# Kernel tuning notes

Hardware: AMD Instinct MI355X
Metric: run time of the kernel (lower is better)

## Reference

```python
import jax, jax.numpy as jnp
import numpy as np
from jax import lax

DN = ('NCHW', 'OIHW', 'NCHW')

def _winit(key, fan_in, shape):
    return (jax.random.uniform(key, shape) - 0.5) * 2 * 2.4 / fan_in ** 0.5

def setup_inputs() -> dict:
    key = jax.random.key(0)
    ks = jax.random.split(key, 6)
    B = 131072
    x = jax.random.normal(ks[0], (B, 1, 16, 16), dtype=jnp.float32)
    H1w = _winit(ks[1], 5 * 5 * 1, (12, 1, 5, 5))
    H1b = jnp.zeros((12, 8, 8), jnp.float32)
    H2w = _winit(ks[2], 5 * 5 * 8, (12, 8, 5, 5))
    H2b = jnp.zeros((12, 4, 4), jnp.float32)
    H3w = _winit(ks[3], 4 * 4 * 12, (4 * 4 * 12, 30))
    H3b = jnp.zeros((30,), jnp.float32)
    outw = _winit(ks[4], 30, (30, 10))
    outb = jnp.zeros((10,), jnp.float32)
    return {"x": x, "H1w": H1w, "H1b": H1b, "H2w": H2w, "H2b": H2b,
            "H3w": H3w, "H3b": H3b, "outw": outw, "outb": outb}

def _pad_m1(x):
    # constant pad of 2 on H and W with value -1.0
    return jnp.pad(x, ((0, 0), (0, 0), (2, 2), (2, 2)), constant_values=-1.0)

def _conv_s2(x, w):
    return lax.conv_general_dilated(x, w, window_strides=(2, 2),
                                    padding='VALID', dimension_numbers=DN)

def reference(x, H1w, H1b, H2w, H2b, H3w, H3b, outw, outb):
    # eval mode: no roll augmentation, dropout is identity
    x = _pad_m1(x)                                   # [B,1,20,20]
    x = _conv_s2(x, H1w) + H1b                       # [B,12,8,8]
    x = jax.nn.relu(x)
    x = _pad_m1(x)                                   # [B,12,12,12]
    s1 = _conv_s2(x[:, 0:8], H2w[0:4])               # [B,4,4,4]
    s2 = _conv_s2(x[:, 4:12], H2w[4:8])              # [B,4,4,4]
    s3 = _conv_s2(jnp.concatenate((x[:, 0:4], x[:, 8:12]), axis=1), H2w[8:12])
    x = jnp.concatenate((s1, s2, s3), axis=1) + H2b  # [B,12,4,4]
    x = jax.nn.relu(x)
    x = x.reshape(x.shape[0], -1)                    # [B,192]
    x = jax.nn.relu(x @ H3w + H3b)                   # [B,30]
    return x @ outw + outb                           # [B,10]
```

## Files before the change

### kernel.cpp

```cpp
#include <hip/hip_runtime.h>
#include <hip/hip_fp16.h>

typedef _Float16 f16x8 __attribute__((ext_vector_type(8)));
typedef float f32x4 __attribute__((ext_vector_type(4)));

union U4H8 { uint4 u; f16x8 h; };
__device__ inline f16x8 asH(uint4 u){ U4H8 x; x.u = u; return x.h; }
__device__ inline unsigned int pk(float a, float b){
    __half2 h = __floats2half2_rn(a, b);
    union { __half2 h; unsigned int u; } c; c.h = h; return c.u;
}
__device__ inline unsigned int pkr(float a, float b){
    return pk(fmaxf(a, 0.f), fmaxf(b, 0.f));
}
__device__ inline unsigned short h16(float a){
    union { __half h; unsigned short s; } c; c.h = __float2half(a); return c.s;
}

#define NFRAG 28
#define WS_B1 7168
#define WS_B2 8192
#define WS_B3 8448
#define WS_B4 8960

__global__ __launch_bounds__(256) void build_tables(
    const float* __restrict__ H1w, const float* __restrict__ H1b,
    const float* __restrict__ H2w, const float* __restrict__ H2b,
    const float* __restrict__ H3w, const float* __restrict__ H3b,
    const float* __restrict__ outw, const float* __restrict__ outb,
    unsigned int* __restrict__ ws)
{
    const int t = threadIdx.x, b = blockIdx.x;
    float* wsf = (float*)ws;

    if (b < NFRAG) {
        if (t < 64) {
            const int lane = t, ch = lane >> 4, oc = lane & 15;
            const int fi = b;
            unsigned short us[8];
            for (int j = 0; j < 8; ++j) {
                float w = 0.f;
                if (fi < 2) {
                    int kh = fi * 4 + ch;
                    if (kh < 5 && j < 5 && oc < 12) w = H1w[oc * 25 + kh * 5 + j];
                } else if (fi < 15) {
                    int kk = fi - 2;
                    int tap = kk * 2 + (ch >> 1);
                    int ic = (ch & 1) * 8 + j;
                    if (tap < 25 && oc < 12) {
                        int kh = tap / 5, kw = tap % 5;
                        int q = oc >> 2, icl = -1;
                        if (q == 0)      { if (ic < 8) icl = ic; }
                        else if (q == 1) { if (ic >= 4 && ic < 12) icl = ic - 4; }
                        else             { if (ic < 4) icl = ic;
                                           else if (ic >= 8 && ic < 12) icl = ic - 4; }
                        if (icl >= 0) w = H2w[((oc * 8 + icl) * 5 + kh) * 5 + kw];
                    }
                } else if (fi < 27) {
                    int idx = fi - 15, nt = idx / 6, kk = idx % 6;
                    int k = kk * 32 + ch * 8 + j;
                    int pos = k / 12, oc2 = k % 12;
                    int col = nt * 16 + oc;
                    if (col < 30) w = H3w[(oc2 * 16 + pos) * 30 + col];
                } else {
                    int k = ch * 8 + j;
                    if (k < 30 && oc < 10) w = outw[k * 10 + oc];
                }
                us[j] = h16(w);
            }
            uint4 u;
            u.x = us[0] | ((unsigned int)us[1] << 16);
            u.y = us[2] | ((unsigned int)us[3] << 16);
            u.z = us[4] | ((unsigned int)us[5] << 16);
            u.w = us[6] | ((unsigned int)us[7] << 16);
            ((uint4*)ws)[fi * 64 + lane] = u;
        }
    } else if (b == NFRAG) {
        for (int idx = t; idx < 1024; idx += 256) {
            int e = idx >> 6, l2 = idx & 63;
            int tt = e >> 2, r = e & 3;
            int oc = 4 * (l2 >> 4) + r, m2 = l2 & 15;
            int oh = 2 * tt + (m2 >> 3), ow = m2 & 7;
            float v = 0.f;
            if (oc < 12) {
                v = H1b[oc * 64 + oh * 8 + ow];
                for (int kh = 0; kh < 5; ++kh)
                    for (int kw = 0; kw < 5; ++kw) {
                        int rr = 2 * oh + kh, cc = 2 * ow + kw;
                        if (rr < 2 || rr >= 18 || cc < 2 || cc >= 18)
                            v -= H1w[oc * 25 + kh * 5 + kw];
                    }
            }
            wsf[WS_B1 + e * 64 + l2] = v;
        }
    } else {
        {
            int e = t >> 6, l2 = t & 63;
            int oc = 4 * (l2 >> 4) + e, m2 = l2 & 15;
            int oh = m2 >> 2, ow = m2 & 3;
            float v = 0.f;
            if (oc < 12) {
                v = H2b[oc * 16 + oh * 4 + ow];
                for (int icl = 0; icl < 8; ++icl)
                    for (int kh = 0; kh < 5; ++kh)
                        for (int kw = 0; kw < 5; ++kw) {
                            int rr = 2 * oh + kh - 2, cc = 2 * ow + kw - 2;
                            if (rr < 0 || rr >= 8 || cc < 0 || cc >= 8)
                                v -= H2w[((oc * 8 + icl) * 5 + kh) * 5 + kw];
                        }
            }
            wsf[WS_B2 + e * 64 + l2] = v;
        }
        for (int i = t; i < 512; i += 256) {
            int e = i >> 6, l2 = i & 63;
            int nt = e >> 2, r = e & 3, ch = l2 >> 4;
            int j = nt * 16 + 4 * ch + r;
            wsf[WS_B3 + e * 64 + l2] = (j < 30) ? H3b[j] : 0.f;
        }
        {
            int e = t >> 6, l2 = t & 63, ch = l2 >> 4;
            int j = 4 * ch + e;
            wsf[WS_B4 + e * 64 + l2] = (j < 10) ? outb[j] : 0.f;
        }
    }
}

#define H2B 18432
#define H3B 21504
__global__ __launch_bounds__(256, 4) void modernnet_mfma(
    const float* __restrict__ x, const unsigned int* __restrict__ ws,
    float* __restrict__ out)
{
    __shared__ uint4 lds4[1376];
    char* L = (char*)lds4;
    const int t = threadIdx.x, wave = t >> 6, l = t & 63;
    const int ch = l >> 4, m = l & 15;
    char* base = L + wave * 4608;
    const int sblk = blockIdx.x * 8;
    const int s0 = sblk + wave * 2;

    const uint4* fr = (const uint4*)ws;
    const float* wsf = (const float*)ws;

    float4 xv0 = *(const float4*)(x + (size_t)(s0 + 0) * 256 + l * 4);
    float4 xv1 = *(const float4*)(x + (size_t)(s0 + 1) * 256 + l * 4);

    uint4 c1b0 = fr[0 * 64 + l], c1b1 = fr[1 * 64 + l];
    f32x4 b1f[4];
    #pragma unroll
    for (int tt = 0; tt < 4; ++tt)
        #pragma unroll
        for (int r = 0; r < 4; ++r) b1f[tt][r] = wsf[WS_B1 + (tt * 4 + r) * 64 + l];

    int c2off[13];
    {
        const int mb = 24 * (m >> 2) + 2 * (m & 3);
        const int hb = (ch & 1) << 4;
        const int sel = (ch >> 1) & 1;
        #pragma unroll
        for (int kk = 0; kk < 13; ++kk) {
            const int t0 = 2 * kk;
            const int t1 = (2 * kk + 1 <= 24) ? 2 * kk + 1 : 24;
            const int p0 = (t0 / 5) * 12 + (t0 % 5);
            const int p1 = (t1 / 5) * 12 + (t1 % 5);
            int pos = mb + (sel ? p1 : p0);
            c2off[kk] = ((pos << 5) + hb) ^ ((pos & 12) << 2);
        }
    }

    uint4 c2b[13];
    #pragma unroll
    for (int kk = 0; kk < 13; ++kk) c2b[kk] = fr[(2 + kk) * 64 + l];
    f32x4 b2f;
    #pragma unroll
    for (int r = 0; r < 4; ++r) b2f[r] = wsf[WS_B2 + r * 64 + l];

    #pragma unroll
    for (int s = 0; s < 2; ++s) {
        {
            uint4 z; z.x = z.y = z.z = z.w = 0u;
            if (l < 60) ((uint4*)base)[l] = z;
        }
        {
            const float4 v = (s == 0) ? xv0 : xv1;
            const int r = l >> 2, c = (l & 3) * 4;
            char* dst = base + (r + 2) * 48 + (c + 2) * 2;
            ((unsigned int*)dst)[0] = pk(v.x, v.y);
            ((unsigned int*)dst)[1] = pk(v.z, v.w);
        }

        uint4 rd[5];
        #pragma unroll
        for (int i = 0; i < 5; ++i) {
            const int cho = (i < 4) ? ch * 48 : 0;
            const unsigned int* p = (const unsigned int*)
                (base + (2 * i + (m >> 3)) * 96 + (m & 7) * 4 + cho);
            rd[i] = make_uint4(p[0], p[1], p[2], p[3]);
        }
        f32x4 acc1[4];
        #pragma unroll
        for (int tt = 0; tt < 4; ++tt) {
            f32x4 acc = b1f[tt];
            acc = __builtin_amdgcn_mfma_f32_16x16x32_f16(asH(c1b0), asH(rd[tt]), acc, 0, 0, 0);
            acc = __builtin_amdgcn_mfma_f32_16x16x32_f16(asH(c1b1), asH(rd[tt + 1]), acc, 0, 0, 0);
            acc1[tt] = acc;
        }

        #pragma unroll
        for (int tt = 0; tt < 4; ++tt) {
            const int pos = (2 * tt + (m >> 3) + 2) * 12 + (m & 7) + 2;
            const int off = ((pos << 5) + ch * 8) ^ ((pos & 12) << 2);
            unsigned int w0 = pkr(acc1[tt][0], acc1[tt][1]);
            unsigned int w1 = pkr(acc1[tt][2], acc1[tt][3]);
            *(uint2*)(base + off) = make_uint2(w0, w1);
        }

        {
            uint4 z; z.x = z.y = z.z = z.w = 0u;
            #pragma unroll
            for (int k2 = 0; k2 < 3; ++k2) {
                int idx = l + k2 * 64;
                if (idx < 160) {
                    int pi = idx >> 1, half = idx & 1;
                    int pos;
                    if (pi < 24) pos = pi;
                    else if (pi < 48) pos = pi + 96;
                    else {
                        int q = pi - 48;
                        int c = q & 3; c = (c < 2) ? c : c + 8;
                        pos = (2 + (q >> 2)) * 12 + c;
                    }
                    int off = ((pos << 5) + (half << 4)) ^ ((pos & 12) << 2);
                    *(uint4*)(base + off) = z;
                }
            }
        }

        {
            f32x4 a = b2f;
            #pragma unroll
            for (int kk = 0; kk < 13; ++kk) {
                uint4 r0 = *(const uint4*)(base + c2off[kk]);
                a = __builtin_amdgcn_mfma_f32_16x16x32_f16(asH(c2b[kk]), asH(r0), a, 0, 0, 0);
            }
            if (ch < 3) {
                const int slot = wave * 2 + s;
                const int off = m * 24 + ch * 8;
                unsigned int w0 = pkr(a[0], a[1]);
                unsigned int w1 = pkr(a[2], a[3]);
                *(uint2*)(L + H2B + slot * 384 + (off ^ (slot << 4))) = make_uint2(w0, w1);
            }
        }
    }

    uint4 afc[6];
    if (wave < 2) {
        #pragma unroll
        for (int kk = 0; kk < 6; ++kk) afc[kk] = fr[(15 + wave * 6 + kk) * 64 + l];
    }

    __syncthreads();

    if (wave < 2) {
        const int nt = wave;
        const int slot = m & 7;
        f32x4 acc;
        #pragma unroll
        for (int r = 0; r < 4; ++r) acc[r] = wsf[WS_B3 + (nt * 4 + r) * 64 + l];
        #pragma unroll
        for (int kk = 0; kk < 6; ++kk) {
            uint4 bb = *(const uint4*)(L + H2B + slot * 384 +
                                       ((kk * 64 + ch * 16) ^ (slot << 4)));
            acc = __builtin_amdgcn_mfma_f32_16x16x32_f16(asH(afc[kk]), asH(bb), acc, 0, 0, 0);
        }
        if (m < 8) {
            unsigned int w0 = pkr(acc[0], acc[1]);
            unsigned int w1 = pkr(acc[2], acc[3]);
            *(uint2*)(L + H3B + m * 64 + nt * 32 + ch * 8) = make_uint2(w0, w1);
        }
    }

    __syncthreads();

    if (wave == 0) {
        uint4 aw = fr[27 * 64 + l];
        uint4 bb = *(const uint4*)(L + H3B + (m & 7) * 64 + ch * 16);
        f32x4 acc;
        #pragma unroll
        for (int r = 0; r < 4; ++r) acc[r] = wsf[WS_B4 + r * 64 + l];
        acc = __builtin_amdgcn_mfma_f32_16x16x32_f16(asH(aw), asH(bb), acc, 0, 0, 0);
        if (m < 8) {
            float* op = out + (size_t)(sblk + m) * 10 + 4 * ch;
            if (ch < 2) {
                *(float2*)op       = make_float2(acc[0], acc[1]);
                *(float2*)(op + 2) = make_float2(acc[2], acc[3]);
            } else if (ch == 2) {
                *(float2*)op       = make_float2(acc[0], acc[1]);
            }
        }
    }
}

extern "C" void kernel_launch(void* const* d_in, const int* in_sizes, int n_in,
                              void* d_out, int out_size, void* d_ws, size_t ws_size,
                              hipStream_t stream) {
    const float* x    = (const float*)d_in[0];
    const float* H1w  = (const float*)d_in[1];
    const float* H1b  = (const float*)d_in[2];
    const float* H2w  = (const float*)d_in[3];
    const float* H2b  = (const float*)d_in[4];
    const float* H3w  = (const float*)d_in[5];
    const float* H3b  = (const float*)d_in[6];
    const float* outw = (const float*)d_in[7];
    const float* outb = (const float*)d_in[8];
    float* outp = (float*)d_out;
    unsigned int* ws = (unsigned int*)d_ws;

    build_tables<<<30, 256, 0, stream>>>(H1w, H1b, H2w, H2b, H3w, H3b, outw, outb, ws);

    const int B = in_sizes[0] / 256;
    const int blocks = B / 8;
    modernnet_mfma<<<blocks, 256, 0, stream>>>(x, ws, outp);
}
```

Before: 102.2 us.

## Double block to 16 samples, batch conv1 for both samples, fill FC MFMA columns

```diff
diff --git a/kernel.cpp b/kernel.cpp
--- a/kernel.cpp
+++ b/kernel.cpp
@@ -125,25 +125,27 @@
     }
 }
 
-#define H2B 18432
-#define H3B 21504
-__global__ __launch_bounds__(256, 4) void modernnet_mfma(
+#define XS1B 36864
+#define H3B3 44544
+__global__ __launch_bounds__(512, 4) void modernnet_mfma(
     const float* __restrict__ x, const unsigned int* __restrict__ ws,
     float* __restrict__ out)
 {
-    __shared__ uint4 lds4[1376];
+    __shared__ uint4 lds4[2848];
     char* L = (char*)lds4;
     const int t = threadIdx.x, wave = t >> 6, l = t & 63;
     const int ch = l >> 4, m = l & 15;
     char* base = L + wave * 4608;
-    const int sblk = blockIdx.x * 8;
+    char* x1b  = L + XS1B + wave * 960;
+    const int sblk = blockIdx.x * 16;
     const int s0 = sblk + wave * 2;
 
     const uint4* fr = (const uint4*)ws;
     const float* wsf = (const float*)ws;
 
-    float4 xv0 = *(const float4*)(x + (size_t)(s0 + 0) * 256 + l * 4);
-    float4 xv1 = *(const float4*)(x + (size_t)(s0 + 1) * 256 + l * 4);
+    const float* xp = x + (size_t)s0 * 256 + l * 8;
+    float4 xv0 = *(const float4*)xp;
+    float4 xv1 = *(const float4*)(xp + 4);
 
     uint4 c1b0 = fr[0 * 64 + l], c1b1 = fr[1 * 64 + l];
     f32x4 b1f[4];
@@ -168,6 +170,45 @@
         }
     }
 
+    {
+        uint4 z; z.x = z.y = z.z = z.w = 0u;
+        if (l < 60) {
+            ((uint4*)base)[l] = z;
+            ((uint4*)x1b)[l] = z;
+        }
+    }
+
+    {
+        int sI = l >> 5, idx = l & 31;
+        int r = idx >> 1, c = (idx & 1) * 8;
+        char* dst = (sI ? x1b : base) + (r + 2) * 48 + (c + 2) * 2;
+        ((unsigned int*)dst)[0] = pk(xv0.x, xv0.y);
+        ((unsigned int*)dst)[1] = pk(xv0.z, xv0.w);
+        ((unsigned int*)dst)[2] = pk(xv1.x, xv1.y);
+        ((unsigned int*)dst)[3] = pk(xv1.z, xv1.w);
+    }
+
+    uint4 rd[2][5];
+    #pragma unroll
+    for (int s = 0; s < 2; ++s)
+        #pragma unroll
+        for (int i = 0; i < 5; ++i) {
+            const int cho = (i < 4) ? ch * 48 : 0;
+            const char* src = (s ? x1b : base)
+                + (2 * i + (m >> 3)) * 96 + (m & 7) * 4 + cho;
+            const unsigned int* p = (const unsigned int*)src;
+            rd[s][i] = make_uint4(p[0], p[1], p[2], p[3]);
+        }
+    f32x4 acc1[8];
+    #pragma unroll
+    for (int i = 0; i < 8; ++i) {
+        const int s = i >> 2, tt = i & 3;
+        f32x4 acc = b1f[tt];
+        acc = __builtin_amdgcn_mfma_f32_16x16x32_f16(asH(c1b0), asH(rd[s][tt]), acc, 0, 0, 0);
+        acc = __builtin_amdgcn_mfma_f32_16x16x32_f16(asH(c1b1), asH(rd[s][tt + 1]), acc, 0, 0, 0);
+        acc1[i] = acc;
+    }
+
     uint4 c2b[13];
     #pragma unroll
     for (int kk = 0; kk < 13; ++kk) c2b[kk] = fr[(2 + kk) * 64 + l];
@@ -177,41 +218,13 @@
 
     #pragma unroll
     for (int s = 0; s < 2; ++s) {
-        {
-            uint4 z; z.x = z.y = z.z = z.w = 0u;
-            if (l < 60) ((uint4*)base)[l] = z;
-        }
-        {
-            const float4 v = (s == 0) ? xv0 : xv1;
-            const int r = l >> 2, c = (l & 3) * 4;
-            char* dst = base + (r + 2) * 48 + (c + 2) * 2;
-            ((unsigned int*)dst)[0] = pk(v.x, v.y);
-            ((unsigned int*)dst)[1] = pk(v.z, v.w);
-        }
-
-        uint4 rd[5];
-        #pragma unroll
-        for (int i = 0; i < 5; ++i) {
-            const int cho = (i < 4) ? ch * 48 : 0;
-            const unsigned int* p = (const unsigned int*)
-                (base + (2 * i + (m >> 3)) * 96 + (m & 7) * 4 + cho);
-            rd[i] = make_uint4(p[0], p[1], p[2], p[3]);
-        }
-        f32x4 acc1[4];
         #pragma unroll
         for (int tt = 0; tt < 4; ++tt) {
-            f32x4 acc = b1f[tt];
-            acc = __builtin_amdgcn_mfma_f32_16x16x32_f16(asH(c1b0), asH(rd[tt]), acc, 0, 0, 0);
-            acc = __builtin_amdgcn_mfma_f32_16x16x32_f16(asH(c1b1), asH(rd[tt + 1]), acc, 0, 0, 0);
-            acc1[tt] = acc;
-        }
-
-        #pragma unroll
-        for (int tt = 0; tt < 4; ++tt) {
+            const f32x4 acc = acc1[s * 4 + tt];
             const int pos = (2 * tt + (m >> 3) + 2) * 12 + (m & 7) + 2;
             const int off = ((pos << 5) + ch * 8) ^ ((pos & 12) << 2);
-            unsigned int w0 = pkr(acc1[tt][0], acc1[tt][1]);
-            unsigned int w1 = pkr(acc1[tt][2], acc1[tt][3]);
+            unsigned int w0 = pkr(acc[0], acc[1]);
+            unsigned int w1 = pkr(acc[2], acc[3]);
             *(uint2*)(base + off) = make_uint2(w0, w1);
         }
 
@@ -248,8 +261,13 @@
                 const int off = m * 24 + ch * 8;
                 unsigned int w0 = pkr(a[0], a[1]);
                 unsigned int w1 = pkr(a[2], a[3]);
-                *(uint2*)(L + H2B + slot * 384 + (off ^ (slot << 4))) = make_uint2(w0, w1);
-            }
+                *(uint2*)(x1b + s * 384 + (off ^ ((slot & 7) << 4))) = make_uint2(w0, w1);
+            }
+        }
+
+        if (s == 0) {
+            uint4 z; z.x = z.y = z.z = z.w = 0u;
+            (void)z;
         }
     }
 
@@ -263,33 +281,32 @@
 
     if (wave < 2) {
         const int nt = wave;
-        const int slot = m & 7;
         f32x4 acc;
         #pragma unroll
         for (int r = 0; r < 4; ++r) acc[r] = wsf[WS_B3 + (nt * 4 + r) * 64 + l];
         #pragma unroll
         for (int kk = 0; kk < 6; ++kk) {
-            uint4 bb = *(const uint4*)(L + H2B + slot * 384 +
-                                       ((kk * 64 + ch * 16) ^ (slot << 4)));
+            uint4 bb = *(const uint4*)(L + XS1B + (m >> 1) * 960 + (m & 1) * 384 +
+                                       ((kk * 64 + ch * 16) ^ ((m & 7) << 4)));
             acc = __builtin_amdgcn_mfma_f32_16x16x32_f16(asH(afc[kk]), asH(bb), acc, 0, 0, 0);
         }
-        if (m < 8) {
-            unsigned int w0 = pkr(acc[0], acc[1]);
-            unsigned int w1 = pkr(acc[2], acc[3]);
-            *(uint2*)(L + H3B + m * 64 + nt * 32 + ch * 8) = make_uint2(w0, w1);
-        }
+        unsigned int w0 = pkr(acc[0], acc[1]);
+        unsigned int w1 = pkr(acc[2], acc[3]);
+        *(uint2*)(L + H3B3 + m * 64 + ((nt * 32 + ch * 8) ^ ((m & 3) << 4))) =
+            make_uint2(w0, w1);
     }
 
     __syncthreads();
 
     if (wave == 0) {
         uint4 aw = fr[27 * 64 + l];
-        uint4 bb = *(const uint4*)(L + H3B + (m & 7) * 64 + ch * 16);
+        uint4 bb = *(const uint4*)(L + H3B3 + m * 64 +
+                                   ((ch * 16) ^ ((m & 3) << 4)));
         f32x4 acc;
         #pragma unroll
         for (int r = 0; r < 4; ++r) acc[r] = wsf[WS_B4 + r * 64 + l];
         acc = __builtin_amdgcn_mfma_f32_16x16x32_f16(asH(aw), asH(bb), acc, 0, 0, 0);
-        if (m < 8) {
+        {
             float* op = out + (size_t)(sblk + m) * 10 + 4 * ch;
             if (ch < 2) {
                 *(float2*)op       = make_float2(acc[0], acc[1]);
@@ -319,6 +336,6 @@
     build_tables<<<30, 256, 0, stream>>>(H1w, H1b, H2w, H2b, H3w, H3b, outw, outb, ws);
 
     const int B = in_sizes[0] / 256;
-    const int blocks = B / 8;
-    modernnet_mfma<<<blocks, 256, 0, stream>>>(x, ws, outp);
-}
+    const int blocks = B / 16;
+    modernnet_mfma<<<blocks, 512, 0, stream>>>(x, ws, outp);
+}
```

Result: faster. 91.21 us (-10.7%).

## Load conv1 operands directly from global, double block to 16 samples

Applied to the files above, without the earlier changes.

```diff
diff --git a/kernel.cpp b/kernel.cpp
--- a/kernel.cpp
+++ b/kernel.cpp
@@ -125,25 +125,22 @@
     }
 }
 
-#define H2B 18432
-#define H3B 21504
-__global__ __launch_bounds__(256, 4) void modernnet_mfma(
+#define H2B 36864
+#define H3B 43008
+__global__ __launch_bounds__(512, 4) void modernnet_mfma(
     const float* __restrict__ x, const unsigned int* __restrict__ ws,
     float* __restrict__ out)
 {
-    __shared__ uint4 lds4[1376];
+    __shared__ uint4 lds4[2752];
     char* L = (char*)lds4;
     const int t = threadIdx.x, wave = t >> 6, l = t & 63;
     const int ch = l >> 4, m = l & 15;
     char* base = L + wave * 4608;
-    const int sblk = blockIdx.x * 8;
+    const int sblk = blockIdx.x * 16;
     const int s0 = sblk + wave * 2;
 
     const uint4* fr = (const uint4*)ws;
     const float* wsf = (const float*)ws;
-
-    float4 xv0 = *(const float4*)(x + (size_t)(s0 + 0) * 256 + l * 4);
-    float4 xv1 = *(const float4*)(x + (size_t)(s0 + 1) * 256 + l * 4);
 
     uint4 c1b0 = fr[0 * 64 + l], c1b1 = fr[1 * 64 + l];
     f32x4 b1f[4];
@@ -175,28 +172,58 @@
     #pragma unroll
     for (int r = 0; r < 4; ++r) b2f[r] = wsf[WS_B2 + r * 64 + l];
 
+    {
+        uint4 z; z.x = z.y = z.z = z.w = 0u;
+        #pragma unroll
+        for (int k2 = 0; k2 < 3; ++k2) {
+            int idx = l + k2 * 64;
+            if (idx < 160) {
+                int pi = idx >> 1, half = idx & 1;
+                int pos;
+                if (pi < 24) pos = pi;
+                else if (pi < 48) pos = pi + 96;
+                else {
+                    int q = pi - 48;
+                    int c = q & 3; c = (c < 2) ? c : c + 8;
+                    pos = (2 + (q >> 2)) * 12 + c;
+                }
+                int off = ((pos << 5) + (half << 4)) ^ ((pos & 12) << 2);
+                *(uint4*)(base + off) = z;
+            }
+        }
+    }
+
+    const int h2r = 2 * (m >> 3);
+    const int c0 = 2 * (m & 7);
+    bool cok[4];
+    #pragma unroll
+    for (int p = 0; p < 4; ++p) {
+        int cA = c0 + 2 * p;
+        cok[p] = (cA >= 2) && (cA <= 16);
+    }
+
     #pragma unroll
     for (int s = 0; s < 2; ++s) {
-        {
-            uint4 z; z.x = z.y = z.z = z.w = 0u;
-            if (l < 60) ((uint4*)base)[l] = z;
-        }
-        {
-            const float4 v = (s == 0) ? xv0 : xv1;
-            const int r = l >> 2, c = (l & 3) * 4;
-            char* dst = base + (r + 2) * 48 + (c + 2) * 2;
-            ((unsigned int*)dst)[0] = pk(v.x, v.y);
-            ((unsigned int*)dst)[1] = pk(v.z, v.w);
-        }
+        const float* xg = x + (size_t)(s0 + s) * 256;
 
         uint4 rd[5];
         #pragma unroll
         for (int i = 0; i < 5; ++i) {
-            const int cho = (i < 4) ? ch * 48 : 0;
-            const unsigned int* p = (const unsigned int*)
-                (base + (2 * i + (m >> 3)) * 96 + (m & 7) * 4 + cho);
-            rd[i] = make_uint4(p[0], p[1], p[2], p[3]);
-        }
+            const int r = 4 * i + h2r + ch;
+            const bool rok = (r >= 2) && (r <= 17);
+            const int gb = (r - 2) * 16 + (c0 - 2);
+            unsigned int wd[4];
+            #pragma unroll
+            for (int p = 0; p < 4; ++p) {
+                int gi = gb + 2 * p;
+                gi = gi < 0 ? 0 : (gi > 254 ? 254 : gi);
+                float2 v = *(const float2*)(xg + gi);
+                const bool ok = rok && cok[p];
+                wd[p] = ok ? pk(v.x, v.y) : 0u;
+            }
+            rd[i] = make_uint4(wd[0], wd[1], wd[2], wd[3]);
+        }
+
         f32x4 acc1[4];
         #pragma unroll
         for (int tt = 0; tt < 4; ++tt) {
@@ -216,27 +243,6 @@
         }
 
         {
-            uint4 z; z.x = z.y = z.z = z.w = 0u;
-            #pragma unroll
-            for (int k2 = 0; k2 < 3; ++k2) {
-                int idx = l + k2 * 64;
-                if (idx < 160) {
-                    int pi = idx >> 1, half = idx & 1;
-                    int pos;
-                    if (pi < 24) pos = pi;
-                    else if (pi < 48) pos = pi + 96;
-                    else {
-                        int q = pi - 48;
-                        int c = q & 3; c = (c < 2) ? c : c + 8;
-                        pos = (2 + (q >> 2)) * 12 + c;
-                    }
-                    int off = ((pos << 5) + (half << 4)) ^ ((pos & 12) << 2);
-                    *(uint4*)(base + off) = z;
-                }
-            }
-        }
-
-        {
             f32x4 a = b2f;
             #pragma unroll
             for (int kk = 0; kk < 13; ++kk) {
@@ -248,7 +254,7 @@
                 const int off = m * 24 + ch * 8;
                 unsigned int w0 = pkr(a[0], a[1]);
                 unsigned int w1 = pkr(a[2], a[3]);
-                *(uint2*)(L + H2B + slot * 384 + (off ^ (slot << 4))) = make_uint2(w0, w1);
+                *(uint2*)(L + H2B + slot * 384 + (off ^ ((slot & 7) << 4))) = make_uint2(w0, w1);
             }
         }
     }
@@ -263,33 +269,32 @@
 
     if (wave < 2) {
         const int nt = wave;
-        const int slot = m & 7;
         f32x4 acc;
         #pragma unroll
         for (int r = 0; r < 4; ++r) acc[r] = wsf[WS_B3 + (nt * 4 + r) * 64 + l];
         #pragma unroll
         for (int kk = 0; kk < 6; ++kk) {
-            uint4 bb = *(const uint4*)(L + H2B + slot * 384 +
-                                       ((kk * 64 + ch * 16) ^ (slot << 4)));
+            uint4 bb = *(const uint4*)(L + H2B + m * 384 +
+                                       ((kk * 64 + ch * 16) ^ ((m & 7) << 4)));
             acc = __builtin_amdgcn_mfma_f32_16x16x32_f16(asH(afc[kk]), asH(bb), acc, 0, 0, 0);
         }
-        if (m < 8) {
-            unsigned int w0 = pkr(acc[0], acc[1]);
-            unsigned int w1 = pkr(acc[2], acc[3]);
-            *(uint2*)(L + H3B + m * 64 + nt * 32 + ch * 8) = make_uint2(w0, w1);
-        }
+        unsigned int w0 = pkr(acc[0], acc[1]);
+        unsigned int w1 = pkr(acc[2], acc[3]);
+        *(uint2*)(L + H3B + m * 64 + ((nt * 32 + ch * 8) ^ ((m & 3) << 4))) =
+            make_uint2(w0, w1);
     }
 
     __syncthreads();
 
     if (wave == 0) {
         uint4 aw = fr[27 * 64 + l];
-        uint4 bb = *(const uint4*)(L + H3B + (m & 7) * 64 + ch * 16);
+        uint4 bb = *(const uint4*)(L + H3B + m * 64 +
+                                   ((ch * 16) ^ ((m & 3) << 4)));
         f32x4 acc;
         #pragma unroll
         for (int r = 0; r < 4; ++r) acc[r] = wsf[WS_B4 + r * 64 + l];
         acc = __builtin_amdgcn_mfma_f32_16x16x32_f16(asH(aw), asH(bb), acc, 0, 0, 0);
-        if (m < 8) {
+        {
             float* op = out + (size_t)(sblk + m) * 10 + 4 * ch;
             if (ch < 2) {
                 *(float2*)op       = make_float2(acc[0], acc[1]);
@@ -319,6 +324,6 @@
     build_tables<<<30, 256, 0, stream>>>(H1w, H1b, H2w, H2b, H3w, H3b, outw, outb, ws);
 
     const int B = in_sizes[0] / 256;
-    const int blocks = B / 8;
-    modernnet_mfma<<<blocks, 256, 0, stream>>>(x, ws, outp);
-}
+    const int blocks = B / 16;
+    modernnet_mfma<<<blocks, 512, 0, stream>>>(x, ws, outp);
+}
```

After: 333.7 us. 227% more time.
